# Performance work log

Hardware: AMD Instinct MI355X
Metric: run time of the kernel (lower is better)

The kernel has to match this reference:

```python
import jax, jax.numpy as jnp
import numpy as np

POOL = (7, 7)          # pool_size from init
CROP = (14, 14)        # crop_size = [p*2 for p in pool_size]


def setup_inputs() -> dict:
    key = jax.random.key(0)
    kf, kxy, kwh = jax.random.split(key, 3)
    H_img, W_img = 800, 800
    feature = jax.random.normal(kf, (1, 50, 50, 512), dtype=jnp.float32)
    N = 1024
    # valid boxes: x1<x2, y1<y2, inside the 800x800 image
    xy1 = jax.random.uniform(kxy, (N, 2), minval=0.0, maxval=600.0)
    wh = jax.random.uniform(kwh, (N, 2), minval=32.0, maxval=200.0)
    xy2 = jnp.clip(xy1 + wh, 0.0, 799.0)
    rois = jnp.concatenate([xy1[:, 0:1], xy1[:, 1:2], xy2[:, 0:1], xy2[:, 1:2]], axis=1)  # (x1,y1,x2,y2)
    img_size = jnp.array([H_img, W_img], dtype=jnp.int32)  # (H, W)
    return {"feature": feature, "rois": rois, "img_size": img_size}


def _roi_pool(feature, rois, img_size):
    H, W = feature.shape[1], feature.shape[2]
    ch, cw = CROP
    ih = img_size[0].astype(jnp.float32)
    iw = img_size[1].astype(jnp.float32)
    # normalize rois (x1,y1,x2,y2) by [W,H,W,H], reorder to (y1,x1,y2,x2)
    x1 = rois[:, 0] / iw
    y1 = rois[:, 1] / ih
    x2 = rois[:, 2] / iw
    y2 = rois[:, 3] / ih
    # TF crop_and_resize sampling grid (crop size > 1 branch)
    gy = jnp.arange(ch, dtype=jnp.float32)
    gx = jnp.arange(cw, dtype=jnp.float32)
    in_y = y1[:, None] * (H - 1) + gy[None, :] * ((y2 - y1) * (H - 1) / (ch - 1))[:, None]  # [N,ch]
    in_x = x1[:, None] * (W - 1) + gx[None, :] * ((x2 - x1) * (W - 1) / (cw - 1))[:, None]  # [N,cw]
    top = jnp.floor(in_y)
    left = jnp.floor(in_x)
    ly = in_y - top   # [N,ch]
    lx = in_x - left  # [N,cw]
    t = jnp.clip(top, 0, H - 1).astype(jnp.int32)
    b = jnp.clip(top + 1, 0, H - 1).astype(jnp.int32)
    l = jnp.clip(left, 0, W - 1).astype(jnp.int32)
    r = jnp.clip(left + 1, 0, W - 1).astype(jnp.int32)
    img = feature[0]  # box_ind is all zeros -> single image [H,W,C]
    tl = img[t[:, :, None], l[:, None, :]]  # [N,ch,cw,C]
    tr = img[t[:, :, None], r[:, None, :]]
    bl = img[b[:, :, None], l[:, None, :]]
    br = img[b[:, :, None], r[:, None, :]]
    lyE = ly[:, :, None, None]
    lxE = lx[:, None, :, None]
    crops = (tl * (1 - lyE) * (1 - lxE) + tr * (1 - lyE) * lxE
             + bl * lyE * (1 - lxE) + br * lyE * lxE)
    # extrapolation_value = 0 outside [0, dim-1]
    valid = (((in_y >= 0) & (in_y <= H - 1))[:, :, None]
             & ((in_x >= 0) & (in_x <= W - 1))[:, None, :])
    crops = jnp.where(valid[..., None], crops, 0.0)
    # 2x2 max pool, stride 2 (crop dims are even so SAME == VALID)
    N, C = crops.shape[0], crops.shape[-1]
    pooled = crops.reshape(N, ch // 2, 2, cw // 2, 2, C).max(axis=(2, 4))  # [N,7,7,C]
    return pooled


def reference(feature, rois, img_size):
    return _roi_pool(feature, rois, img_size)
```

## Files before the change

kernel.cpp:

```cpp
#include <hip/hip_runtime.h>

#define FH 50
#define FW 50
#define FC 512
#define NROI 1024
#define ROWPITCH (FW * FC)

__device__ __forceinline__ float4 lerp4(float4 a, float4 b, float t) {
    float4 r;
    r.x = fmaf(t, b.x - a.x, a.x);
    r.y = fmaf(t, b.y - a.y, a.y);
    r.z = fmaf(t, b.z - a.z, a.z);
    r.w = fmaf(t, b.w - a.w, a.w);
    return r;
}

__device__ __forceinline__ float4 max44(float4 a, float4 b) {
    float4 r;
    r.x = fmaxf(a.x, b.x);
    r.y = fmaxf(a.y, b.y);
    r.z = fmaxf(a.z, b.z);
    r.w = fmaxf(a.w, b.w);
    return r;
}

__global__ __launch_bounds__(256) void roi_pool_kernel(
    const float* __restrict__ feature,
    const float* __restrict__ rois,
    const int*   __restrict__ img_size,
    float*       __restrict__ out)
{
    int wid  = (blockIdx.x * 256 + threadIdx.x) >> 6;
    wid = __builtin_amdgcn_readfirstlane(wid);
    int lane = threadIdx.x & 63;

    int n    = wid / 14;
    int rem  = wid - n * 14;
    int py   = rem >> 1;
    int half = rem & 1;

    float ih = (float)img_size[0];
    float iw = (float)img_size[1];
    const float* rp = rois + (size_t)n * 4;
    float x1 = rp[0] / iw, y1 = rp[1] / ih, x2 = rp[2] / iw, y2 = rp[3] / ih;

    const float HM1 = 49.0f, WM1 = 49.0f;
    float sy = (y2 - y1) * HM1 / 13.0f;
    float sx = (x2 - x1) * WM1 / 13.0f;
    float oy = y1 * HM1;
    float ox = x1 * WM1;

    float iy0 = oy + (float)(2 * py)     * sy;
    float iy1 = oy + (float)(2 * py + 1) * sy;
    float fy0 = floorf(iy0), fy1 = floorf(iy1);
    float ly0 = iy0 - fy0,   ly1 = iy1 - fy1;
    int t0 = min(max((int)fy0, 0), FH - 1);
    int b0 = min(max((int)fy0 + 1, 0), FH - 1);
    int t1 = min(max((int)fy1, 0), FH - 1);
    int b1 = min(max((int)fy1 + 1, 0), FH - 1);
    bool vy0 = (iy0 >= 0.0f) && (iy0 <= HM1);
    bool vy1 = (iy1 >= 0.0f) && (iy1 <= HM1);
    bool sameRows = (t1 == t0) && (b1 == b0);

    const float* fbase = feature + half * 256 + lane * 4;

    auto loadcol = [&](int c, float4& V0, float4& V1) {
        c = min(max(c, 0), FW - 1);
        const float* p = fbase + (size_t)c * FC;
        float4 A = *reinterpret_cast<const float4*>(p + (size_t)t0 * ROWPITCH);
        float4 B = *reinterpret_cast<const float4*>(p + (size_t)b0 * ROWPITCH);
        V0 = lerp4(A, B, ly0);
        if (sameRows) {
            V1 = lerp4(A, B, ly1);
        } else {
            float4 C = *reinterpret_cast<const float4*>(p + (size_t)t1 * ROWPITCH);
            float4 D = *reinterpret_cast<const float4*>(p + (size_t)b1 * ROWPITCH);
            V1 = lerp4(C, D, ly1);
        }
    };

    float4 VA0, VA1, VB0, VB1;
    int curL = (int)floorf(ox);
    loadcol(curL,     VA0, VA1);
    loadcol(curL + 1, VB0, VB1);

    float* obase = out + ((size_t)n * 49 + (size_t)py * 7) * FC + half * 256 + lane * 4;

    float4 m = make_float4(0.f, 0.f, 0.f, 0.f);
#pragma unroll 2
    for (int j = 0; j < 14; ++j) {
        float ix = ox + (float)j * sx;
        float fx = floorf(ix);
        int   lj = (int)fx;
        float lx = ix - fx;
        while (lj > curL) {
            ++curL;
            VA0 = VB0; VA1 = VB1;
            loadcol(curL + 1, VB0, VB1);
        }
        float4 s0 = lerp4(VA0, VB0, lx);
        float4 s1 = lerp4(VA1, VB1, lx);
        bool vx = (ix >= 0.0f) && (ix <= WM1);
        if (!(vx && vy0)) s0 = make_float4(0.f, 0.f, 0.f, 0.f);
        if (!(vx && vy1)) s1 = make_float4(0.f, 0.f, 0.f, 0.f);
        float4 s = max44(s0, s1);
        if (j & 1) {
            m = max44(m, s);
            __builtin_nontemporal_store(m.x, &obase[(size_t)(j >> 1) * FC + 0]);
            __builtin_nontemporal_store(m.y, &obase[(size_t)(j >> 1) * FC + 1]);
            __builtin_nontemporal_store(m.z, &obase[(size_t)(j >> 1) * FC + 2]);
            __builtin_nontemporal_store(m.w, &obase[(size_t)(j >> 1) * FC + 3]);
        } else {
            m = s;
        }
    }
}

extern "C" void kernel_launch(void* const* d_in, const int* in_sizes, int n_in,
                              void* d_out, int out_size, void* d_ws, size_t ws_size,
                              hipStream_t stream) {
    const float* feature  = (const float*)d_in[0];
    const float* rois     = (const float*)d_in[1];
    const int*   img_size = (const int*)d_in[2];
    float* out = (float*)d_out;

    int blocks = NROI * 14 / 4;
    roi_pool_kernel<<<blocks, 256, 0, stream>>>(feature, rois, img_size, out);
}
```

Baseline: 36.94 us.

## Software-pipeline column loads with two-slot prefetch and vector nontemporal stores

Replaces the lazy column-advance loop with an explicit walk over the column range the ROI touches. Loads for the next two columns stay in flight while the current column is interpolated and consumed, hiding global-load latency. Output stores become single 128-bit nontemporal vector stores instead of four scalar ones. The cost is higher register pressure from the two prefetch slots and more complex control flow. Correctness now depends on the precomputed column count matching the per-sample floor indices, including the clamp at the right edge.

```diff
diff --git a/kernel.cpp b/kernel.cpp
--- a/kernel.cpp
+++ b/kernel.cpp
@@ -5,6 +5,8 @@
 #define FC 512
 #define NROI 1024
 #define ROWPITCH (FW * FC)
+
+typedef float f4v __attribute__((ext_vector_type(4)));
 
 __device__ __forceinline__ float4 lerp4(float4 a, float4 b, float t) {
     float4 r;
@@ -62,58 +64,77 @@
     bool vy1 = (iy1 >= 0.0f) && (iy1 <= HM1);
     bool sameRows = (t1 == t0) && (b1 == b0);
 
+    int c0u   = (int)floorf(ox);
+    int lumax = (int)floorf(ox + 13.0f * sx);
+    int ncols = lumax + 2 - c0u;
+
     const float* fbase = feature + half * 256 + lane * 4;
-
-    auto loadcol = [&](int c, float4& V0, float4& V1) {
-        c = min(max(c, 0), FW - 1);
-        const float* p = fbase + (size_t)c * FC;
-        float4 A = *reinterpret_cast<const float4*>(p + (size_t)t0 * ROWPITCH);
-        float4 B = *reinterpret_cast<const float4*>(p + (size_t)b0 * ROWPITCH);
-        V0 = lerp4(A, B, ly0);
-        if (sameRows) {
-            V1 = lerp4(A, B, ly1);
-        } else {
-            float4 C = *reinterpret_cast<const float4*>(p + (size_t)t1 * ROWPITCH);
-            float4 D = *reinterpret_cast<const float4*>(p + (size_t)b1 * ROWPITCH);
-            V1 = lerp4(C, D, ly1);
-        }
-    };
-
-    float4 VA0, VA1, VB0, VB1;
-    int curL = (int)floorf(ox);
-    loadcol(curL,     VA0, VA1);
-    loadcol(curL + 1, VB0, VB1);
-
     float* obase = out + ((size_t)n * 49 + (size_t)py * 7) * FC + half * 256 + lane * 4;
 
+#define ISSUE(slot, A, B, C, D)                                                   \
+    {                                                                             \
+        int cc = min(c0u + (slot), FW - 1);                                       \
+        const float* p = fbase + (size_t)cc * FC;                                 \
+        A = *reinterpret_cast<const float4*>(p + (size_t)t0 * ROWPITCH);          \
+        B = *reinterpret_cast<const float4*>(p + (size_t)b0 * ROWPITCH);          \
+        if (!sameRows) {                                                          \
+            C = *reinterpret_cast<const float4*>(p + (size_t)t1 * ROWPITCH);      \
+            D = *reinterpret_cast<const float4*>(p + (size_t)b1 * ROWPITCH);      \
+        }                                                                         \
+    }
+
+    float4 p0A, p0B, p0C, p0D;
+    float4 p1A, p1B, p1C, p1D;
+    ISSUE(0, p0A, p0B, p0C, p0D);
+    ISSUE(1, p1A, p1B, p1C, p1D);
+
+    float4 Vp0, Vp1;
     float4 m = make_float4(0.f, 0.f, 0.f, 0.f);
-#pragma unroll 2
-    for (int j = 0; j < 14; ++j) {
-        float ix = ox + (float)j * sx;
-        float fx = floorf(ix);
-        int   lj = (int)fx;
-        float lx = ix - fx;
-        while (lj > curL) {
-            ++curL;
-            VA0 = VB0; VA1 = VB1;
-            loadcol(curL + 1, VB0, VB1);
+    int j = 0;
+
+#define CONSUME(scol)                                                             \
+    while (j < 14) {                                                              \
+        float ix = ox + (float)j * sx;                                            \
+        float fx = floorf(ix);                                                    \
+        if ((int)fx != (scol) + c0u - 1) break;                                   \
+        float lx = ix - fx;                                                       \
+        float4 s0 = lerp4(Vp0, Vc0, lx);                                          \
+        float4 s1 = lerp4(Vp1, Vc1, lx);                                          \
+        bool vx = (ix >= 0.0f) && (ix <= WM1);                                    \
+        if (!(vx && vy0)) s0 = make_float4(0.f, 0.f, 0.f, 0.f);                   \
+        if (!(vx && vy1)) s1 = make_float4(0.f, 0.f, 0.f, 0.f);                   \
+        float4 sm = max44(s0, s1);                                                \
+        if (j & 1) {                                                              \
+            m = max44(m, sm);                                                     \
+            __builtin_nontemporal_store(*reinterpret_cast<f4v*>(&m),              \
+                reinterpret_cast<f4v*>(obase + (size_t)(j >> 1) * FC));           \
+        } else {                                                                  \
+            m = sm;                                                               \
+        }                                                                         \
+        ++j;                                                                      \
+    }
+
+    for (int s = 0; s < ncols; s += 2) {
+        {
+            float4 rA = p0A, rB = p0B, rC = p0C, rD = p0D;
+            if (s + 2 < ncols) ISSUE(s + 2, p0A, p0B, p0C, p0D);
+            float4 Vc0 = lerp4(rA, rB, ly0);
+            float4 Vc1 = sameRows ? lerp4(rA, rB, ly1) : lerp4(rC, rD, ly1);
+            if (s >= 1) { CONSUME(s); }
+            Vp0 = Vc0; Vp1 = Vc1;
         }
-        float4 s0 = lerp4(VA0, VB0, lx);
-        float4 s1 = lerp4(VA1, VB1, lx);
-        bool vx = (ix >= 0.0f) && (ix <= WM1);
-        if (!(vx && vy0)) s0 = make_float4(0.f, 0.f, 0.f, 0.f);
-        if (!(vx && vy1)) s1 = make_float4(0.f, 0.f, 0.f, 0.f);
-        float4 s = max44(s0, s1);
-        if (j & 1) {
-            m = max44(m, s);
-            __builtin_nontemporal_store(m.x, &obase[(size_t)(j >> 1) * FC + 0]);
-            __builtin_nontemporal_store(m.y, &obase[(size_t)(j >> 1) * FC + 1]);
-            __builtin_nontemporal_store(m.z, &obase[(size_t)(j >> 1) * FC + 2]);
-            __builtin_nontemporal_store(m.w, &obase[(size_t)(j >> 1) * FC + 3]);
-        } else {
-            m = s;
+        if (s + 1 < ncols) {
+            float4 rA = p1A, rB = p1B, rC = p1C, rD = p1D;
+            if (s + 3 < ncols) ISSUE(s + 3, p1A, p1B, p1C, p1D);
+            float4 Vc0 = lerp4(rA, rB, ly0);
+            float4 Vc1 = sameRows ? lerp4(rA, rB, ly1) : lerp4(rC, rD, ly1);
+            CONSUME(s + 1);
+            Vp0 = Vc0; Vp1 = Vc1;
         }
     }
+
+#undef ISSUE
+#undef CONSUME
 }
 
 extern "C" void kernel_launch(void* const* d_in, const int* in_sizes, int n_in,
```

Measured after the change: 37.05 us. Within noise of the previous version (+0.3%).

## Assign each wave a whole ROI channel quarter and reuse vertical interpolations across rows

Applied to the files above, without the earlier changes.

Each wave now handles one ROI across all 14 sample rows for a 128-channel slice (float2 per lane), rather than one output row for 256 channels. For every feature column it loads each distinct feature row once, builds the vertically interpolated values for all 14 rows, and keeps the previous column so that sampled columns and rows shared between pool rows are loaded only once. This cuts redundant global loads and index arithmetic, but each wave now holds about 28 float2 arrays in registers, uses narrower 8-byte accesses, and the grid shrinks from 3584 to 1024 blocks, so occupancy and latency hiding may drop.

```diff
diff --git a/kernel.cpp b/kernel.cpp
--- a/kernel.cpp
+++ b/kernel.cpp
@@ -6,21 +6,19 @@
 #define NROI 1024
 #define ROWPITCH (FW * FC)
 
-__device__ __forceinline__ float4 lerp4(float4 a, float4 b, float t) {
-    float4 r;
+typedef float f2v __attribute__((ext_vector_type(2)));
+
+__device__ __forceinline__ float2 lerp2(float2 a, float2 b, float t) {
+    float2 r;
     r.x = fmaf(t, b.x - a.x, a.x);
     r.y = fmaf(t, b.y - a.y, a.y);
-    r.z = fmaf(t, b.z - a.z, a.z);
-    r.w = fmaf(t, b.w - a.w, a.w);
     return r;
 }
 
-__device__ __forceinline__ float4 max44(float4 a, float4 b) {
-    float4 r;
+__device__ __forceinline__ float2 max22(float2 a, float2 b) {
+    float2 r;
     r.x = fmaxf(a.x, b.x);
     r.y = fmaxf(a.y, b.y);
-    r.z = fmaxf(a.z, b.z);
-    r.w = fmaxf(a.w, b.w);
     return r;
 }
 
@@ -34,10 +32,8 @@
     wid = __builtin_amdgcn_readfirstlane(wid);
     int lane = threadIdx.x & 63;
 
-    int n    = wid / 14;
-    int rem  = wid - n * 14;
-    int py   = rem >> 1;
-    int half = rem & 1;
+    int n = wid >> 2;
+    int q = wid & 3;
 
     float ih = (float)img_size[0];
     float iw = (float)img_size[1];
@@ -50,70 +46,87 @@
     float oy = y1 * HM1;
     float ox = x1 * WM1;
 
-    float iy0 = oy + (float)(2 * py)     * sy;
-    float iy1 = oy + (float)(2 * py + 1) * sy;
-    float fy0 = floorf(iy0), fy1 = floorf(iy1);
-    float ly0 = iy0 - fy0,   ly1 = iy1 - fy1;
-    int t0 = min(max((int)fy0, 0), FH - 1);
-    int b0 = min(max((int)fy0 + 1, 0), FH - 1);
-    int t1 = min(max((int)fy1, 0), FH - 1);
-    int b1 = min(max((int)fy1 + 1, 0), FH - 1);
-    bool vy0 = (iy0 >= 0.0f) && (iy0 <= HM1);
-    bool vy1 = (iy1 >= 0.0f) && (iy1 <= HM1);
-    bool sameRows = (t1 == t0) && (b1 == b0);
+    int   advmask = 0;
+    int   vymask  = 0;
+    int   rowoff[14];
+    float lyA[14];
+    int   r0 = 0, t_prev = 0;
+#pragma unroll
+    for (int i = 0; i < 14; ++i) {
+        float iy = oy + (float)i * sy;
+        float fy = floorf(iy);
+        int   ti = (int)fy;
+        lyA[i] = iy - fy;
+        if ((iy >= 0.0f) && (iy <= HM1)) vymask |= (1 << i);
+        if (i == 0) r0 = ti;
+        else if (ti > t_prev) advmask |= (1 << i);
+        rowoff[i] = min(max(ti + 1, 0), FH - 1) * ROWPITCH;
+        t_prev = ti;
+    }
+    int proff = min(max(r0, 0), FH - 1) * ROWPITCH;
 
-    const float* fbase = feature + half * 256 + lane * 4;
+    int c0u   = (int)floorf(ox);
+    int lumax = (int)floorf(ox + 13.0f * sx);
+    int ncols = lumax + 2 - c0u;
 
-    auto loadcol = [&](int c, float4& V0, float4& V1) {
-        c = min(max(c, 0), FW - 1);
-        const float* p = fbase + (size_t)c * FC;
-        float4 A = *reinterpret_cast<const float4*>(p + (size_t)t0 * ROWPITCH);
-        float4 B = *reinterpret_cast<const float4*>(p + (size_t)b0 * ROWPITCH);
-        V0 = lerp4(A, B, ly0);
-        if (sameRows) {
-            V1 = lerp4(A, B, ly1);
-        } else {
-            float4 C = *reinterpret_cast<const float4*>(p + (size_t)t1 * ROWPITCH);
-            float4 D = *reinterpret_cast<const float4*>(p + (size_t)b1 * ROWPITCH);
-            V1 = lerp4(C, D, ly1);
+    const float* fq = feature + q * 128 + lane * 2;
+
+    float2 Vp[14], Vc[14], m[7];
+    int j = 0;
+
+#define VERTCOL(colidx, V)                                                      \
+    {                                                                           \
+        const float* colp = fq + (size_t)min(max((colidx), 0), FW - 1) * FC;    \
+        float2 P = *reinterpret_cast<const float2*>(colp + proff);              \
+        float2 C = *reinterpret_cast<const float2*>(colp + rowoff[0]);          \
+        V[0] = lerp2(P, C, lyA[0]);                                             \
+        _Pragma("unroll")                                                       \
+        for (int i = 1; i < 14; ++i) {                                          \
+            if ((advmask >> i) & 1) {                                           \
+                P = C;                                                          \
+                C = *reinterpret_cast<const float2*>(colp + rowoff[i]);         \
+            }                                                                   \
+            V[i] = lerp2(P, C, lyA[i]);                                         \
+        }                                                                       \
+    }
+
+    VERTCOL(c0u, Vp);
+
+    for (int s = 1; s < ncols; ++s) {
+        VERTCOL(c0u + s, Vc);
+
+        int ccolm1 = c0u + s - 1;
+        while (j < 14) {
+            float ix = ox + (float)j * sx;
+            float fx = floorf(ix);
+            if ((int)fx != ccolm1) break;
+            float lx = ix - fx;
+            bool  vx = (ix >= 0.0f) && (ix <= WM1);
+#pragma unroll
+            for (int k = 0; k < 7; ++k) {
+                float2 s0 = lerp2(Vp[2 * k],     Vc[2 * k],     lx);
+                float2 s1 = lerp2(Vp[2 * k + 1], Vc[2 * k + 1], lx);
+                if (!(vx && ((vymask >> (2 * k)) & 1)))     { s0.x = 0.f; s0.y = 0.f; }
+                if (!(vx && ((vymask >> (2 * k + 1)) & 1))) { s1.x = 0.f; s1.y = 0.f; }
+                float2 sm = max22(s0, s1);
+                m[k] = (j & 1) ? max22(m[k], sm) : sm;
+            }
+            if (j & 1) {
+#pragma unroll
+                for (int k = 0; k < 7; ++k) {
+                    float* po = out + ((size_t)n * 49 + (size_t)k * 7 + (size_t)(j >> 1)) * FC
+                                    + q * 128 + lane * 2;
+                    __builtin_nontemporal_store(*reinterpret_cast<f2v*>(&m[k]),
+                                                reinterpret_cast<f2v*>(po));
+                }
+            }
+            ++j;
         }
-    };
 
-    float4 VA0, VA1, VB0, VB1;
-    int curL = (int)floorf(ox);
-    loadcol(curL,     VA0, VA1);
-    loadcol(curL + 1, VB0, VB1);
-
-    float* obase = out + ((size_t)n * 49 + (size_t)py * 7) * FC + half * 256 + lane * 4;
-
-    float4 m = make_float4(0.f, 0.f, 0.f, 0.f);
-#pragma unroll 2
-    for (int j = 0; j < 14; ++j) {
-        float ix = ox + (float)j * sx;
-        float fx = floorf(ix);
-        int   lj = (int)fx;
-        float lx = ix - fx;
-        while (lj > curL) {
-            ++curL;
-            VA0 = VB0; VA1 = VB1;
-            loadcol(curL + 1, VB0, VB1);
-        }
-        float4 s0 = lerp4(VA0, VB0, lx);
-        float4 s1 = lerp4(VA1, VB1, lx);
-        bool vx = (ix >= 0.0f) && (ix <= WM1);
-        if (!(vx && vy0)) s0 = make_float4(0.f, 0.f, 0.f, 0.f);
-        if (!(vx && vy1)) s1 = make_float4(0.f, 0.f, 0.f, 0.f);
-        float4 s = max44(s0, s1);
-        if (j & 1) {
-            m = max44(m, s);
-            __builtin_nontemporal_store(m.x, &obase[(size_t)(j >> 1) * FC + 0]);
-            __builtin_nontemporal_store(m.y, &obase[(size_t)(j >> 1) * FC + 1]);
-            __builtin_nontemporal_store(m.z, &obase[(size_t)(j >> 1) * FC + 2]);
-            __builtin_nontemporal_store(m.w, &obase[(size_t)(j >> 1) * FC + 3]);
-        } else {
-            m = s;
-        }
+#pragma unroll
+        for (int i = 0; i < 14; ++i) Vp[i] = Vc[i];
     }
+#undef VERTCOL
 }
 
 extern "C" void kernel_launch(void* const* d_in, const int* in_sizes, int n_in,
@@ -124,6 +137,6 @@
     const int*   img_size = (const int*)d_in[2];
     float* out = (float*)d_out;
 
-    int blocks = NROI * 14 / 4;
+    int blocks = NROI;
     roi_pool_kernel<<<blocks, 256, 0, stream>>>(feature, rois, img_size, out);
 }
```

Result: slower. 74.20 us (+100.9%).
